# Performance work log

Measured on AMD Instinct MI355X. Metric: run time of the kernel, lower is better.

Reference implementation:

```python
import jax, jax.numpy as jnp
import numpy as np

NUM_NODES = 100000
EMB_DIM = 64
OUT_C = 64
K = 3
NUM_EDGES = 1600000


def setup_inputs() -> dict:
    key = jax.random.key(0)
    k1, k2, k3, k4 = jax.random.split(key, 4)
    x_indices = jnp.arange(NUM_NODES, dtype=jnp.int64)
    ei = jax.random.randint(k1, (2, NUM_EDGES), 0, NUM_NODES, dtype=jnp.int64)
    # learned params: embedding table + final linear of SGConv
    emb_weight = jax.random.normal(k2, (NUM_NODES, EMB_DIM), dtype=jnp.float32)
    lin_w = jax.random.normal(k3, (OUT_C, EMB_DIM), dtype=jnp.float32) / np.sqrt(EMB_DIM)
    lin_b = jax.random.normal(k4, (OUT_C,), dtype=jnp.float32) * 0.01
    return {"x_indices": x_indices, "ei": ei, "emb_weight": emb_weight,
            "lin_w": lin_w, "lin_b": lin_b}


def _sgconv(x, ei, lin_w, lin_b, k_hops):
    """PyG SGConv: (D^-1/2 (A+I) D^-1/2)^K X, then Linear."""
    n = x.shape[0]
    row, col = ei[0], ei[1]
    loops = jnp.arange(n, dtype=ei.dtype)
    row = jnp.concatenate([row, loops])
    col = jnp.concatenate([col, loops])
    ones = jnp.ones(row.shape[0], dtype=x.dtype)
    deg = jax.ops.segment_sum(ones, col, num_segments=n)  # in-degree incl. self-loops
    dinv = jnp.where(deg > 0, jax.lax.rsqrt(deg), 0.0)
    norm = dinv[row] * dinv[col]  # [E+N]
    for _ in range(k_hops):
        # gather source features, scale, scatter-add to targets
        x = jax.ops.segment_sum(x[row] * norm[:, None], col, num_segments=n)
    return x @ lin_w.T + lin_b


def reference(x_indices, ei, emb_weight, lin_w, lin_b):
    x = emb_weight[x_indices]  # [N, EMB_DIM] embedding lookup
    return _sgconv(x, ei, lin_w, lin_b, K)
```

## Files before the change

### kernel.cpp

```cpp
#include <hip/hip_runtime.h>
#include <hip/hip_bf16.h>
#include <math.h>


#define FLAG_MX 0
#define FLAG_ME 1
#define SH 9
#define WC 512
#define CH 4096
#define RMASK 0x7FFFFFu

using short8 = __attribute__((ext_vector_type(8))) short;
using f32x4 = __attribute__((ext_vector_type(4))) float;

__device__ inline int idx_at(const void* p, long long i, int mode) {
    switch (mode) {
        case 1: return (int)((const long long*)p)[i];
        case 2: return (int)((const float*)p)[i];
        case 3: return (int)((const double*)p)[i];
        default: return ((const int*)p)[i];
    }
}

__device__ inline unsigned short f2bf(float f) {
    union { float f; unsigned u; } v; v.f = f;
    unsigned r = v.u + 0x7FFFu + ((v.u >> 16) & 1u);
    return (unsigned short)(r >> 16);
}
__device__ inline float bflo(unsigned d) { union { unsigned u; float f; } v; v.u = d << 16; return v.f; }
__device__ inline float bfhi(unsigned d) { union { unsigned u; float f; } v; v.u = d & 0xFFFF0000u; return v.f; }
__device__ inline unsigned pk(float a, float b) {
    return (unsigned)f2bf(a) | ((unsigned)f2bf(b) << 16);
}

__device__ int detect_me_block(const void* ei, int n, int* sbuf) {
    int t = threadIdx.x;
    int oke = 15;
    const int* w = (const int*)ei;
    const long long* L = (const long long*)ei;
    const float* f = (const float*)ei;
    const double* d = (const double*)ei;
    for (int k = t; k < 2048; k += 256) {
        if (!((unsigned)w[k] < (unsigned)n)) oke &= ~1;
        long long lv = L[k];
        if (!(lv >= 0 && lv < (long long)n)) oke &= ~2;
        float fv = f[k];
        if (!(fv >= 0.f && fv < (float)n && fv == truncf(fv))) oke &= ~4;
        double dv = d[k];
        if (!(dv >= 0.0 && dv < (double)n && dv == trunc(dv))) oke &= ~8;
    }
    sbuf[t] = oke;
    __syncthreads();
    for (int st = 128; st; st >>= 1) {
        if (t < st) sbuf[t] &= sbuf[t + st];
        __syncthreads();
    }
    int r = sbuf[0];
    __syncthreads();
    return (r & 2) ? 1 : (r & 8) ? 3 : (r & 4) ? 2 : 0;
}

__device__ int detect_mx_block(const void* xidx, int* sbuf) {
    int t = threadIdx.x;
    int okx = 15;
    const int* w = (const int*)xidx;
    const long long* L = (const long long*)xidx;
    const float* f = (const float*)xidx;
    const double* d = (const double*)xidx;
    for (int k = t; k < 2048; k += 256) {
        if (w[k] != k) okx &= ~1;
        if (L[k] != (long long)k) okx &= ~2;
        if (!(f[k] == (float)k)) okx &= ~4;
        if (!(d[k] == (double)k)) okx &= ~8;
    }
    sbuf[t] = okx;
    __syncthreads();
    for (int st = 128; st; st >>= 1) {
        if (t < st) sbuf[t] &= sbuf[t + st];
        __syncthreads();
    }
    int r = sbuf[0];
    __syncthreads();
    return (r & 2) ? 1 : (r & 8) ? 3 : (r & 4) ? 2 : 0;
}

__global__ void __launch_bounds__(256) k_p1(
        const void* __restrict__ ei, const void* __restrict__ xidx,
        long long E, int n, int NBUK, int NBLK,
        int* __restrict__ bhist, int* __restrict__ flags) {
    __shared__ int hist[256];
    __shared__ int sbuf[256];
    int t = threadIdx.x;
    int blk = blockIdx.x;
    int me = detect_me_block(ei, n, sbuf);
    if (blk == 0) {
        int mx = detect_mx_block(xidx, sbuf);
        if (t == 0) { flags[FLAG_ME] = me; flags[FLAG_MX] = mx; }
    }
    long long base = (long long)blk * CH;
    int cnt = (int)min((long long)CH, E - base);
    hist[t] = 0;
    __syncthreads();
    for (int i = t; i < cnt; i += 256) {
        int c = idx_at(ei, E + base + i, me);
        int b = min(c >> SH, NBUK - 1);
        atomicAdd(&hist[b], 1);
    }
    __syncthreads();
    if (t < NBUK) bhist[(size_t)t * NBLK + blk] = hist[t];
}

__global__ void __launch_bounds__(256) k_p2a(
        int* __restrict__ bhist, int* __restrict__ gcount, int NBLK) {
    __shared__ int s[256];
    int b = blockIdx.x;
    int t = threadIdx.x;
    int* row = bhist + (size_t)b * NBLK;
    int carry = 0;
    for (int base = 0; base < NBLK; base += 256) {
        int i = base + t;
        int v = (i < NBLK) ? row[i] : 0;
        s[t] = v;
        __syncthreads();
        for (int st = 1; st < 256; st <<= 1) {
            int add = (t >= st) ? s[t - st] : 0;
            __syncthreads();
            s[t] += add;
            __syncthreads();
        }
        if (i < NBLK) row[i] = carry + s[t] - v;
        int total = s[255];
        __syncthreads();
        carry += total;
    }
    if (t == 0) gcount[b] = carry;
}

__device__ void scan_gcount(const int* gcount, int NBUK, int* p, int* gb_ex) {
    int t = threadIdx.x;
    int v = (t < NBUK) ? gcount[t] : 0;
    p[t] = v;
    __syncthreads();
    for (int st = 1; st < 256; st <<= 1) {
        int add = (t >= st) ? p[t - st] : 0;
        __syncthreads();
        p[t] += add;
        __syncthreads();
    }
    gb_ex[t] = p[t] - v;
    __syncthreads();
}

__device__ void scan_gcount_512(const int* gcount, int NBUK, int* p, int* gb_ex) {
    int t = threadIdx.x;
    int v = (t < 256) ? ((t < NBUK) ? gcount[t] : 0) : 0;
    if (t < 256) p[t] = v;
    __syncthreads();
    for (int st = 1; st < 256; st <<= 1) {
        int add = (t >= st && t < 256) ? p[t - st] : 0;
        __syncthreads();
        if (t < 256) p[t] += add;
        __syncthreads();
    }
    if (t < 256) gb_ex[t] = p[t] - v;
    __syncthreads();
}

__global__ void __launch_bounds__(256) k_p3(
        const void* __restrict__ ei, long long E, int n, int NBUK, int NBLK,
        const int* __restrict__ bhist, const int* __restrict__ gcount,
        unsigned* __restrict__ gstag, const int* __restrict__ flags) {
    __shared__ int hist[256], lbase[256], rsv[256], lcur[256], s[256], gb[256];
    __shared__ unsigned stage[CH];
    int t = threadIdx.x;
    int blk = blockIdx.x;
    scan_gcount(gcount, NBUK, s, gb);
    long long base = (long long)blk * CH;
    int cnt = (int)min((long long)CH, E - base);
    int me = flags[FLAG_ME];
    hist[t] = 0;
    __syncthreads();
    for (int i = t; i < cnt; i += 256) {
        int c = idx_at(ei, E + base + i, me);
        atomicAdd(&hist[min(c >> SH, NBUK - 1)], 1);
    }
    __syncthreads();
    int v = hist[t];
    s[t] = v;
    __syncthreads();
    for (int st = 1; st < 256; st <<= 1) {
        int add = (t >= st) ? s[t - st] : 0;
        __syncthreads();
        s[t] += add;
        __syncthreads();
    }
    lbase[t] = s[t] - v;
    lcur[t] = s[t] - v;
    if (t < NBUK) rsv[t] = gb[t] + bhist[(size_t)t * NBLK + blk];
    __syncthreads();
    for (int i = t; i < cnt; i += 256) {
        long long e = base + i;
        int r = idx_at(ei, e, me);
        int c = idx_at(ei, E + e, me);
        int b = min(c >> SH, NBUK - 1);
        unsigned pkv = ((unsigned)r & RMASK) |
                       (((unsigned)(c - (b << SH)) & (WC - 1)) << 23);
        int slot = atomicAdd(&lcur[b], 1);
        stage[slot] = pkv;
    }
    __syncthreads();
    for (int i = t; i < cnt; i += 256) {
        unsigned pkv = stage[i];
        int lo = 0, hi = NBUK - 1;
        while (lo < hi) {
            int mid = (lo + hi + 1) >> 1;
            if (lbase[mid] <= i) lo = mid; else hi = mid - 1;
        }
        gstag[rsv[lo] + (i - lbase[lo])] = pkv;
    }
}

__global__ void __launch_bounds__(512) k_p4(
        const unsigned* __restrict__ gstag, const int* __restrict__ gcount,
        int* __restrict__ off, float* __restrict__ dinv,
        int* __restrict__ rowidx, int n, int NBUK) {
    __shared__ int hist[WC], lofs[WC], cur[WC], p[512], gb[256];
    int t = threadIdx.x;
    int b = blockIdx.x;
    int cbase = b << SH;
    scan_gcount_512(gcount, NBUK, p, gb);
    int e0 = gb[b];
    int e1 = e0 + gcount[b];
    int cnt = e1 - e0;
    if (b == NBUK - 1 && t == 0) off[n] = e1;
    hist[t] = 0;
    __syncthreads();
    for (int i = t; i < cnt; i += 512) {
        atomicAdd(&hist[gstag[e0 + i] >> 23], 1);
    }
    __syncthreads();
    int v = hist[t];
    p[t] = v;
    __syncthreads();
    for (int st = 1; st < 512; st <<= 1) {
        int add = (t >= st) ? p[t - st] : 0;
        __syncthreads();
        p[t] += add;
        __syncthreads();
    }
    int excl = p[t] - v;
    lofs[t] = excl;
    cur[t] = excl;
    __syncthreads();
    int ncols = n - cbase;
    if (ncols < 0) ncols = 0;
    if (ncols > WC) ncols = WC;
    if (t < ncols) {
        off[cbase + t] = e0 + lofs[t];
        dinv[cbase + t] = rsqrtf((float)(hist[t] + 1));
    }
    for (int i = t; i < cnt; i += 512) {
        unsigned pkv = gstag[e0 + i];
        int cl = (int)(pkv >> 23);
        int slot = atomicAdd(&cur[cl], 1);
        rowidx[e0 + slot] = (int)(pkv & RMASK);
    }
}

__global__ void __launch_bounds__(256) k_z0(
        const void* __restrict__ xidx, const float4* __restrict__ emb4,
        const float* __restrict__ dinv, uint4* __restrict__ z, int n,
        const int* __restrict__ flags) {
    int i = blockIdx.x * 256 + threadIdx.x;
    if (i >= n * 8) return;
    int node = i >> 3, q = i & 7;
    int xi = idx_at(xidx, node, flags[FLAG_MX]);
    if ((unsigned)xi >= (unsigned)n) xi = 0;
    float d = dinv[node];
    float4 a = emb4[(long long)xi * 16 + q * 2];
    float4 b = emb4[(long long)xi * 16 + q * 2 + 1];
    uint4 o;
    o.x = pk(a.x * d, a.y * d);
    o.y = pk(a.z * d, a.w * d);
    o.z = pk(b.x * d, b.y * d);
    o.w = pk(b.z * d, b.w * d);
    z[(long long)node * 8 + q] = o;
}

__device__ inline void acc8(float* acc, uint4 s) {
    acc[0] += bflo(s.x); acc[1] += bfhi(s.x);
    acc[2] += bflo(s.y); acc[3] += bfhi(s.y);
    acc[4] += bflo(s.z); acc[5] += bfhi(s.z);
    acc[6] += bflo(s.w); acc[7] += bfhi(s.w);
}

__global__ void __launch_bounds__(256) k_hop(
        const uint4* __restrict__ zin, uint4* __restrict__ zout,
        const float* __restrict__ dinv, const int* __restrict__ off,
        const int* __restrict__ rowidx, int n, int last) {
    int tid = blockIdx.x * 256 + threadIdx.x;
    int node = tid >> 3;
    int q = tid & 7;
    if (node >= n) return;
    float acc[8];
    {
        uint4 s = zin[(long long)node * 8 + q];
        acc[0] = bflo(s.x); acc[1] = bfhi(s.x);
        acc[2] = bflo(s.y); acc[3] = bfhi(s.y);
        acc[4] = bflo(s.z); acc[5] = bfhi(s.z);
        acc[6] = bflo(s.w); acc[7] = bfhi(s.w);
    }
    int e0 = off[node], e1 = off[node + 1];
    int e = e0;
    for (; e + 4 <= e1; e += 4) {
        int r0 = rowidx[e + 0];
        int r1 = rowidx[e + 1];
        int r2 = rowidx[e + 2];
        int r3 = rowidx[e + 3];
        uint4 s0 = zin[(long long)r0 * 8 + q];
        uint4 s1 = zin[(long long)r1 * 8 + q];
        uint4 s2 = zin[(long long)r2 * 8 + q];
        uint4 s3 = zin[(long long)r3 * 8 + q];
        acc8(acc, s0);
        acc8(acc, s1);
        acc8(acc, s2);
        acc8(acc, s3);
    }
    for (; e < e1; e++) {
        int r = rowidx[e];
        acc8(acc, zin[(long long)r * 8 + q]);
    }
    float d = dinv[node];
    float sc = last ? d : d * d;
    uint4 o;
    o.x = pk(acc[0] * sc, acc[1] * sc);
    o.y = pk(acc[2] * sc, acc[3] * sc);
    o.z = pk(acc[4] * sc, acc[5] * sc);
    o.w = pk(acc[6] * sc, acc[7] * sc);
    zout[(long long)node * 8 + q] = o;
}

__global__ void __launch_bounds__(256) k_lin_mfma(
        const short8* __restrict__ x8, const float* __restrict__ w,
        const float* __restrict__ b, float* __restrict__ out, int n, int ntiles) {
    int lane = threadIdx.x & 63;
    int wv = threadIdx.x >> 6;
    int col = lane & 15, quad = lane >> 4;

    short8 bw[4][2];
#pragma unroll
    for (int tN = 0; tN < 4; tN++)
#pragma unroll
        for (int s = 0; s < 2; s++) {
            const float* src = w + (tN * 16 + col) * 64 + s * 32 + quad * 8;
            short8 v;
#pragma unroll
            for (int j = 0; j < 8; j++) v[j] = (short)f2bf(src[j]);
            bw[tN][s] = v;
        }
    float bv[4];
#pragma unroll
    for (int tN = 0; tN < 4; tN++) bv[tN] = b[tN * 16 + col];

    int tile = blockIdx.x * 4 + wv;
    if (tile >= ntiles) return;
    int node0 = tile * 16;

    short8 a[2];
    int m = node0 + col;
#pragma unroll
    for (int s = 0; s < 2; s++) {
        if (m < n) a[s] = x8[(size_t)m * 8 + s * 4 + quad];
        else a[s] = short8{0, 0, 0, 0, 0, 0, 0, 0};
    }
#pragma unroll
    for (int tN = 0; tN < 4; tN++) {
        f32x4 acc = {bv[tN], bv[tN], bv[tN], bv[tN]};
        acc = __builtin_amdgcn_mfma_f32_16x16x32_bf16(a[0], bw[tN][0], acc, 0, 0, 0);
        acc = __builtin_amdgcn_mfma_f32_16x16x32_bf16(a[1], bw[tN][1], acc, 0, 0, 0);
#pragma unroll
        for (int r = 0; r < 4; r++) {
            int node = node0 + quad * 4 + r;
            if (node < n) out[(size_t)node * 64 + tN * 16 + col] = acc[r];
        }
    }
}

extern "C" void kernel_launch(void* const* d_in, const int* in_sizes, int n_in,
                              void* d_out, int out_size, void* d_ws, size_t ws_size,
                              hipStream_t stream) {
    const void* xidx = d_in[0];
    const void* ei = d_in[1];
    const float* emb = (const float*)d_in[2];
    const float* w = (const float*)d_in[3];
    const float* b = (const float*)d_in[4];

    const int n = in_sizes[0];
    const long long E = in_sizes[1] / 2;
    int NBUK = (int)((n + WC - 1) >> SH);
    if (NBUK > 256) NBUK = 256;
    const int NBLK = (int)((E + CH - 1) / CH);

    char* p = (char*)d_ws;
    auto alloc = [&](size_t bytes) -> void* {
        void* r = (void*)p;
        p += (bytes + 255) & ~(size_t)255;
        return r;
    };
    int* flags = (int*)alloc(256);
    float* dinv = (float*)alloc((size_t)n * 4);
    int* off = (int*)alloc((size_t)(n + 1) * 4);
    int* gcount = (int*)alloc(257 * 4);
    int* bhist = (int*)alloc((size_t)NBLK * NBUK * 4);
    int* rowidx = (int*)alloc((size_t)E * 4);
    uint4* zA = (uint4*)alloc((size_t)n * 64 * 2);
    uint4* zS = (uint4*)d_out;

    unsigned* gstag;
    if ((size_t)E * 4 <= (size_t)n * 64 * 2)
        gstag = (unsigned*)((char*)d_out + (size_t)n * 64 * 2);
    else
        gstag = (unsigned*)alloc((size_t)E * 4);

    k_p1<<<NBLK, 256, 0, stream>>>(ei, xidx, E, n, NBUK, NBLK, bhist, flags);
    k_p2a<<<NBUK, 256, 0, stream>>>(bhist, gcount, NBLK);
    k_p3<<<NBLK, 256, 0, stream>>>(ei, E, n, NBUK, NBLK, bhist, gcount, gstag, flags);
    k_p4<<<NBUK, 512, 0, stream>>>(gstag, gcount, off, dinv, rowidx, n, NBUK);

    const int gF = (n * 8 + 255) / 256;
    const int ntiles = (n + 15) / 16;
    const int gM = (ntiles + 3) / 4;

    k_z0<<<gF, 256, 0, stream>>>(xidx, (const float4*)emb, dinv, zS, n, flags);
    k_hop<<<gF, 256, 0, stream>>>(zS, zA, dinv, off, rowidx, n, 0);
    k_hop<<<gF, 256, 0, stream>>>(zA, zS, dinv, off, rowidx, n, 0);
    k_hop<<<gF, 256, 0, stream>>>(zS, zA, dinv, off, rowidx, n, 1);
    k_lin_mfma<<<gM, 256, 0, stream>>>((const short8*)zA, w, b, (float*)d_out,
                                       n, ntiles);
}
```

Measured before the change: 260.4 us.

## Fuse final hop with MFMA linear layer and precompute bf16 weights

The third propagation hop and the output linear layer now run in one kernel: each block aggregates 32 nodes into swizzled shared memory, then runs MFMA on them directly. This avoids writing and re-reading the bf16 intermediate and drops one kernel launch. The weight conversion to bf16 is moved into an extra block of the prefix-scan kernel, so per-block float-to-bf16 conversion in the linear stage goes away. Buffer ping-pong is reordered so the last hop reads zA while d_out is free for the final output.

Result: faster. 250.5 us (-3.8%).

```diff
diff --git a/kernel.cpp b/kernel.cpp
--- a/kernel.cpp
+++ b/kernel.cpp
@@ -111,10 +111,15 @@
 }
 
 __global__ void __launch_bounds__(256) k_p2a(
-        int* __restrict__ bhist, int* __restrict__ gcount, int NBLK) {
+        int* __restrict__ bhist, int* __restrict__ gcount, int NBLK, int NBUK,
+        const float* __restrict__ w, unsigned short* __restrict__ w8) {
     __shared__ int s[256];
     int b = blockIdx.x;
     int t = threadIdx.x;
+    if (b >= NBUK) {
+        for (int i = t; i < 4096; i += 256) w8[i] = f2bf(w[i]);
+        return;
+    }
     int* row = bhist + (size_t)b * NBLK;
     int carry = 0;
     for (int base = 0; base < NBLK; base += 256) {
@@ -297,7 +302,7 @@
 __global__ void __launch_bounds__(256) k_hop(
         const uint4* __restrict__ zin, uint4* __restrict__ zout,
         const float* __restrict__ dinv, const int* __restrict__ off,
-        const int* __restrict__ rowidx, int n, int last) {
+        const int* __restrict__ rowidx, int n) {
     int tid = blockIdx.x * 256 + threadIdx.x;
     int node = tid >> 3;
     int q = tid & 7;
@@ -331,7 +336,7 @@
         acc8(acc, zin[(long long)r * 8 + q]);
     }
     float d = dinv[node];
-    float sc = last ? d : d * d;
+    float sc = d * d;
     uint4 o;
     o.x = pk(acc[0] * sc, acc[1] * sc);
     o.y = pk(acc[2] * sc, acc[3] * sc);
@@ -340,48 +345,81 @@
     zout[(long long)node * 8 + q] = o;
 }
 
-__global__ void __launch_bounds__(256) k_lin_mfma(
-        const short8* __restrict__ x8, const float* __restrict__ w,
-        const float* __restrict__ b, float* __restrict__ out, int n, int ntiles) {
-    int lane = threadIdx.x & 63;
-    int wv = threadIdx.x >> 6;
+__global__ void __launch_bounds__(256) k_hop3_lin(
+        const uint4* __restrict__ zin, const float* __restrict__ dinv,
+        const int* __restrict__ off, const int* __restrict__ rowidx,
+        const unsigned short* __restrict__ w8, const float* __restrict__ bias,
+        float* __restrict__ out, int n) {
+    __shared__ uint4 z3[32][8];
+    int t = threadIdx.x;
+    int l = t >> 3;
+    int q = t & 7;
+    int node = blockIdx.x * 32 + l;
+    uint4 o = {0u, 0u, 0u, 0u};
+    if (node < n) {
+        float acc[8];
+        {
+            uint4 s = zin[(long long)node * 8 + q];
+            acc[0] = bflo(s.x); acc[1] = bfhi(s.x);
+            acc[2] = bflo(s.y); acc[3] = bfhi(s.y);
+            acc[4] = bflo(s.z); acc[5] = bfhi(s.z);
+            acc[6] = bflo(s.w); acc[7] = bfhi(s.w);
+        }
+        int e0 = off[node], e1 = off[node + 1];
+        int e = e0;
+        for (; e + 4 <= e1; e += 4) {
+            int r0 = rowidx[e + 0];
+            int r1 = rowidx[e + 1];
+            int r2 = rowidx[e + 2];
+            int r3 = rowidx[e + 3];
+            uint4 s0 = zin[(long long)r0 * 8 + q];
+            uint4 s1 = zin[(long long)r1 * 8 + q];
+            uint4 s2 = zin[(long long)r2 * 8 + q];
+            uint4 s3 = zin[(long long)r3 * 8 + q];
+            acc8(acc, s0);
+            acc8(acc, s1);
+            acc8(acc, s2);
+            acc8(acc, s3);
+        }
+        for (; e < e1; e++) {
+            int r = rowidx[e];
+            acc8(acc, zin[(long long)r * 8 + q]);
+        }
+        float d = dinv[node];
+        o.x = pk(acc[0] * d, acc[1] * d);
+        o.y = pk(acc[2] * d, acc[3] * d);
+        o.z = pk(acc[4] * d, acc[5] * d);
+        o.w = pk(acc[6] * d, acc[7] * d);
+    }
+    z3[l][q ^ (l & 7)] = o;
+    __syncthreads();
+
+    int lane = t & 63, wv = t >> 6;
+    int tile = wv >> 1;
+    int nh = wv & 1;
     int col = lane & 15, quad = lane >> 4;
-
-    short8 bw[4][2];
-#pragma unroll
-    for (int tN = 0; tN < 4; tN++)
-#pragma unroll
-        for (int s = 0; s < 2; s++) {
-            const float* src = w + (tN * 16 + col) * 64 + s * 32 + quad * 8;
-            short8 v;
-#pragma unroll
-            for (int j = 0; j < 8; j++) v[j] = (short)f2bf(src[j]);
-            bw[tN][s] = v;
-        }
-    float bv[4];
-#pragma unroll
-    for (int tN = 0; tN < 4; tN++) bv[tN] = b[tN * 16 + col];
-
-    int tile = blockIdx.x * 4 + wv;
-    if (tile >= ntiles) return;
-    int node0 = tile * 16;
-
+    int node0 = blockIdx.x * 32 + tile * 16;
+    int ln = tile * 16 + col;
     short8 a[2];
-    int m = node0 + col;
 #pragma unroll
     for (int s = 0; s < 2; s++) {
-        if (m < n) a[s] = x8[(size_t)m * 8 + s * 4 + quad];
-        else a[s] = short8{0, 0, 0, 0, 0, 0, 0, 0};
-    }
+        int c = s * 4 + quad;
+        a[s] = *(const short8*)&z3[ln][c ^ (ln & 7)];
+    }
+    const short8* wp = (const short8*)w8;
 #pragma unroll
-    for (int tN = 0; tN < 4; tN++) {
-        f32x4 acc = {bv[tN], bv[tN], bv[tN], bv[tN]};
-        acc = __builtin_amdgcn_mfma_f32_16x16x32_bf16(a[0], bw[tN][0], acc, 0, 0, 0);
-        acc = __builtin_amdgcn_mfma_f32_16x16x32_bf16(a[1], bw[tN][1], acc, 0, 0, 0);
+    for (int j = 0; j < 2; j++) {
+        int tN = nh * 2 + j;
+        float bv = bias[tN * 16 + col];
+        f32x4 acc4 = {bv, bv, bv, bv};
+        acc4 = __builtin_amdgcn_mfma_f32_16x16x32_bf16(
+            a[0], wp[(tN * 16 + col) * 8 + 0 * 4 + quad], acc4, 0, 0, 0);
+        acc4 = __builtin_amdgcn_mfma_f32_16x16x32_bf16(
+            a[1], wp[(tN * 16 + col) * 8 + 1 * 4 + quad], acc4, 0, 0, 0);
 #pragma unroll
         for (int r = 0; r < 4; r++) {
-            int node = node0 + quad * 4 + r;
-            if (node < n) out[(size_t)node * 64 + tN * 16 + col] = acc[r];
+            int nd = node0 + quad * 4 + r;
+            if (nd < n) out[(size_t)nd * 64 + tN * 16 + col] = acc4[r];
         }
     }
 }
@@ -414,6 +452,7 @@
     int* bhist = (int*)alloc((size_t)NBLK * NBUK * 4);
     int* rowidx = (int*)alloc((size_t)E * 4);
     uint4* zA = (uint4*)alloc((size_t)n * 64 * 2);
+    unsigned short* w8 = (unsigned short*)alloc(4096 * 2);
     uint4* zS = (uint4*)d_out;
 
     unsigned* gstag;
@@ -423,18 +462,16 @@
         gstag = (unsigned*)alloc((size_t)E * 4);
 
     k_p1<<<NBLK, 256, 0, stream>>>(ei, xidx, E, n, NBUK, NBLK, bhist, flags);
-    k_p2a<<<NBUK, 256, 0, stream>>>(bhist, gcount, NBLK);
+    k_p2a<<<NBUK + 1, 256, 0, stream>>>(bhist, gcount, NBLK, NBUK, w, w8);
     k_p3<<<NBLK, 256, 0, stream>>>(ei, E, n, NBUK, NBLK, bhist, gcount, gstag, flags);
     k_p4<<<NBUK, 512, 0, stream>>>(gstag, gcount, off, dinv, rowidx, n, NBUK);
 
     const int gF = (n * 8 + 255) / 256;
-    const int ntiles = (n + 15) / 16;
-    const int gM = (ntiles + 3) / 4;
-
-    k_z0<<<gF, 256, 0, stream>>>(xidx, (const float4*)emb, dinv, zS, n, flags);
-    k_hop<<<gF, 256, 0, stream>>>(zS, zA, dinv, off, rowidx, n, 0);
-    k_hop<<<gF, 256, 0, stream>>>(zA, zS, dinv, off, rowidx, n, 0);
-    k_hop<<<gF, 256, 0, stream>>>(zS, zA, dinv, off, rowidx, n, 1);
-    k_lin_mfma<<<gM, 256, 0, stream>>>((const short8*)zA, w, b, (float*)d_out,
-                                       n, ntiles);
-}
+    const int gL = (n + 31) / 32;
+
+    k_z0<<<gF, 256, 0, stream>>>(xidx, (const float4*)emb, dinv, zA, n, flags);
+    k_hop<<<gF, 256, 0, stream>>>(zA, zS, dinv, off, rowidx, n);
+    k_hop<<<gF, 256, 0, stream>>>(zS, zA, dinv, off, rowidx, n);
+    k_hop3_lin<<<gL, 256, 0, stream>>>(zA, dinv, off, rowidx, w8, b,
+                                       (float*)d_out, n);
+}
```
